# Kernel optimization log

Hardware: AMD Instinct MI355X
Metric: run time of the kernel (lower is better)

Reference implementation:

```python
import jax, jax.numpy as jnp
import numpy as np

B, N, K = 32, 65536, 2  # batch, nodes, residual dim per node


def setup_inputs() -> dict:
    key = jax.random.key(0)
    k0, k1, k2, k3, k4 = jax.random.split(key, 5)
    r = jax.random.normal(k0, (B, N, K), dtype=jnp.float32)
    w = jax.random.uniform(k1, (B, N, 2), dtype=jnp.float32)  # [conf, node_lambda]
    J_p = jax.random.normal(k2, (B, N, K, 6), dtype=jnp.float32)
    J_d = jax.random.normal(k3, (B, N, K, 1), dtype=jnp.float32)
    lmbda = jax.random.uniform(k4, (1, 1, 1), dtype=jnp.float32)
    return {"r": r, "w": w, "J_p": J_p, "J_d": J_d, "lmbda": lmbda}


def reference(r, w, J_p, J_d, lmbda):
    conf = w[..., 0:1][..., None]          # (B,N,1,1)
    node_lambda = w[..., 1:2]              # (B,N,1)

    cJp = conf * J_p                       # (B,N,K,6)
    cJd = conf * J_d                       # (B,N,K,1)

    H_pp = jnp.einsum('bnki,bnkj->bij', J_p, cJp)              # (B,6,6)
    H_pd = jnp.einsum('bnki,bnkj->bnij', J_p, cJd)             # (B,N,6,1)
    H_dd = jnp.einsum('bnk,bnk->bn', J_d[..., 0], cJd[..., 0])[..., None]  # (B,N,1)

    cr = conf[..., 0] * r                  # (B,N,K)
    g_p = jnp.einsum('bnki,bnk->bi', J_p, cr)[..., None]       # (B,6,1)
    g_d = jnp.einsum('bnk,bnk->bn', J_d[..., 0], cr)[..., None]  # (B,N,1)

    eye6 = jnp.eye(6, dtype=r.dtype)[None]                     # (1,6,6)
    H_pp = H_pp + lmbda * eye6
    H_dd = H_dd + lmbda + node_lambda                          # (B,N,1)

    inv_H_dd = 1.0 / (H_dd + 1e-6)                             # (B,N,1)
    H_pd_inv = H_pd * inv_H_dd[..., None]                      # (B,N,6,1)

    # Schur complement: H_eff = H_pp - sum_n H_pd * inv(H_dd) * H_pd^T
    H_eff = H_pp - jnp.einsum('bnik,bnjk->bij', H_pd_inv, H_pd)  # (B,6,6)
    H_eff = 0.5 * (H_eff + jnp.swapaxes(H_eff, -1, -2))
    H_eff = H_eff + 1e-3 * eye6

    g_eff = g_p - jnp.sum(H_pd_inv * g_d[..., None], axis=1)   # (B,6,1)

    delta_pose = jnp.linalg.solve(H_eff, g_eff)                # (B,6,1)

    # back-substitution for depth updates
    v = jnp.einsum('bnik,bi->bnk', H_pd, delta_pose[..., 0])   # (B,N,1)
    delta_depth = inv_H_dd * (g_d - v)                          # (B,N,1)

    return delta_pose[..., 0], delta_depth
```

## Files before the change

### kernel.cpp

```cpp
#include <hip/hip_runtime.h>

#define BN_B 32
#define BN_N 65536
#define BLOCKS_PER_B 64
#define THREADS 256

typedef _Float16 half_t;
struct alignas(16) Half8 { half_t h[8]; };
union StateU { Half8 s; uint4 u; };

#define STATE_OFFSET (256 * 1024)
#define STATE_BYTES ((size_t)BN_B * BN_N * 16)
#define WS_NEEDED (STATE_OFFSET + STATE_BYTES)

__device__ __forceinline__ void point_core(
    const float* __restrict__ r, const float* __restrict__ w,
    const float* __restrict__ J_p, const float* __restrict__ J_d,
    size_t p, float lam,
    float jpa[6], float jpb[6], float& c, float& cr0, float& cr1,
    float hpd[6], float& gd, float& ihdd)
{
    float2 wv = *(const float2*)(w + p * 2);
    float2 rv = *(const float2*)(r + p * 2);
    float2 jd = *(const float2*)(J_d + p * 2);
    float4 jp0 = *(const float4*)(J_p + p * 12);
    float4 jp1 = *(const float4*)(J_p + p * 12 + 4);
    float4 jp2 = *(const float4*)(J_p + p * 12 + 8);
    c = wv.x;
    float nl = wv.y;
    jpa[0] = jp0.x; jpa[1] = jp0.y; jpa[2] = jp0.z; jpa[3] = jp0.w; jpa[4] = jp1.x; jpa[5] = jp1.y;
    jpb[0] = jp1.z; jpb[1] = jp1.w; jpb[2] = jp2.x; jpb[3] = jp2.y; jpb[4] = jp2.z; jpb[5] = jp2.w;
    float cjd0 = c * jd.x, cjd1 = c * jd.y;
#pragma unroll
    for (int i = 0; i < 6; ++i) hpd[i] = jpa[i] * cjd0 + jpb[i] * cjd1;
    float hdd = jd.x * cjd0 + jd.y * cjd1;
    cr0 = c * rv.x; cr1 = c * rv.y;
    gd = jd.x * cr0 + jd.y * cr1;
    ihdd = 1.0f / (hdd + lam + nl + 1e-6f);
}

template <bool WRITE_STATE>
__global__ __launch_bounds__(THREADS) void k_reduce(
    const float* __restrict__ r, const float* __restrict__ w,
    const float* __restrict__ J_p, const float* __restrict__ J_d,
    const float* __restrict__ lmbda, float* __restrict__ partials,
    uint4* __restrict__ state)
{
    const int b = blockIdx.y;
    const int blk = blockIdx.x;
    const float lam = lmbda[0];

    float acc[27];
#pragma unroll
    for (int i = 0; i < 27; ++i) acc[i] = 0.0f;

    const int n0 = blk * (BN_N / BLOCKS_PER_B);
    const int n1 = n0 + (BN_N / BLOCKS_PER_B);
    const size_t baseP = (size_t)b * BN_N;

    for (int n = n0 + (int)threadIdx.x; n < n1; n += THREADS) {
        size_t p = baseP + n;
        float jpa[6], jpb[6], hpd[6];
        float c, cr0, cr1, gd, ihdd;
        point_core(r, w, J_p, J_d, p, lam, jpa, jpb, c, cr0, cr1, hpd, gd, ihdd);

        StateU su;
        int t = 0;
#pragma unroll
        for (int i = 0; i < 6; ++i) {
            float ca = c * jpa[i];
            float cb = c * jpb[i];
            float hs = ihdd * hpd[i];
#pragma unroll
            for (int j = i; j < 6; ++j, ++t)
                acc[t] += ca * jpa[j] + cb * jpb[j] - hs * hpd[j];
            acc[21 + i] += jpa[i] * cr0 + jpb[i] * cr1 - hs * gd;
            if (WRITE_STATE) su.s.h[i] = (half_t)hs;
        }
        if (WRITE_STATE) {
            su.s.h[6] = (half_t)(ihdd * gd);
            su.s.h[7] = (half_t)0.0f;
            state[p] = su.u;
        }
    }

#pragma unroll
    for (int i = 0; i < 27; ++i) {
        float v = acc[i];
#pragma unroll
        for (int off = 32; off > 0; off >>= 1) v += __shfl_down(v, off);
        acc[i] = v;
    }

    __shared__ float red[4][27];
    const int wave = threadIdx.x >> 6;
    const int lane = threadIdx.x & 63;
    if (lane == 0) {
#pragma unroll
        for (int i = 0; i < 27; ++i) red[wave][i] = acc[i];
    }
    __syncthreads();
    if (threadIdx.x < 27) {
        float s = red[0][threadIdx.x] + red[1][threadIdx.x] +
                  red[2][threadIdx.x] + red[3][threadIdx.x];
        partials[((size_t)b * BLOCKS_PER_B + blk) * 27 + threadIdx.x] = s;
    }
}

__global__ void k_solve(const float* __restrict__ partials,
                        const float* __restrict__ lmbda,
                        float* __restrict__ out)
{
    const int b = blockIdx.x;
    __shared__ float sum27[27];
    if (threadIdx.x < 27) {
        float s = 0.0f;
        for (int p = 0; p < BLOCKS_PER_B; ++p)
            s += partials[((size_t)b * BLOCKS_PER_B + p) * 27 + threadIdx.x];
        sum27[threadIdx.x] = s;
    }
    __syncthreads();
    if (threadIdx.x == 0) {
        const float lam = lmbda[0];
        float A[6][7];
        int t = 0;
        for (int i = 0; i < 6; ++i)
            for (int j = i; j < 6; ++j, ++t) { A[i][j] = sum27[t]; A[j][i] = sum27[t]; }
        for (int i = 0; i < 6; ++i) A[i][i] += lam + 0.001f;
        for (int i = 0; i < 6; ++i) A[i][6] = sum27[21 + i];

        for (int col = 0; col < 6; ++col) {
            int piv = col;
            float best = fabsf(A[col][col]);
            for (int rw = col + 1; rw < 6; ++rw) {
                float v = fabsf(A[rw][col]);
                if (v > best) { best = v; piv = rw; }
            }
            if (piv != col) {
                for (int j = 0; j < 7; ++j) {
                    float tmp = A[col][j]; A[col][j] = A[piv][j]; A[piv][j] = tmp;
                }
            }
            float inv = 1.0f / A[col][col];
            for (int rw = col + 1; rw < 6; ++rw) {
                float f = A[rw][col] * inv;
                for (int j = col; j < 7; ++j) A[rw][j] -= f * A[col][j];
            }
        }
        float x[6];
        for (int i = 5; i >= 0; --i) {
            float s = A[i][6];
            for (int j = i + 1; j < 6; ++j) s -= A[i][j] * x[j];
            x[i] = s / A[i][i];
        }
        for (int i = 0; i < 6; ++i) out[b * 6 + i] = x[i];
    }
}

__global__ __launch_bounds__(THREADS) void k_depth2(
    const uint4* __restrict__ state, const float* __restrict__ dp,
    float* __restrict__ out_depth)
{
    const int b = blockIdx.y;
    const int blk = blockIdx.x;
    float d[6];
#pragma unroll
    for (int i = 0; i < 6; ++i) d[i] = dp[b * 6 + i];

    const int n0 = blk * (BN_N / BLOCKS_PER_B);
    const int n1 = n0 + (BN_N / BLOCKS_PER_B);
    const size_t baseP = (size_t)b * BN_N;

    for (int n = n0 + (int)threadIdx.x; n < n1; n += THREADS) {
        size_t p = baseP + n;
        StateU su;
        su.u = state[p];
        float v = 0.0f;
#pragma unroll
        for (int i = 0; i < 6; ++i) v += (float)su.s.h[i] * d[i];
        out_depth[p] = (float)su.s.h[6] - v;
    }
}

__global__ __launch_bounds__(THREADS) void k_depth(
    const float* __restrict__ r, const float* __restrict__ w,
    const float* __restrict__ J_p, const float* __restrict__ J_d,
    const float* __restrict__ lmbda, const float* __restrict__ dp,
    float* __restrict__ out_depth)
{
    const int b = blockIdx.y;
    const int blk = blockIdx.x;
    const float lam = lmbda[0];
    float d0 = dp[b * 6 + 0], d1 = dp[b * 6 + 1], d2 = dp[b * 6 + 2];
    float d3 = dp[b * 6 + 3], d4 = dp[b * 6 + 4], d5 = dp[b * 6 + 5];

    const int n0 = blk * (BN_N / BLOCKS_PER_B);
    const int n1 = n0 + (BN_N / BLOCKS_PER_B);
    const size_t baseP = (size_t)b * BN_N;

    for (int n = n0 + (int)threadIdx.x; n < n1; n += THREADS) {
        size_t p = baseP + n;
        float jpa[6], jpb[6], hpd[6];
        float c, cr0, cr1, gd, ihdd;
        point_core(r, w, J_p, J_d, p, lam, jpa, jpb, c, cr0, cr1, hpd, gd, ihdd);
        float v = hpd[0] * d0 + hpd[1] * d1 + hpd[2] * d2 +
                  hpd[3] * d3 + hpd[4] * d4 + hpd[5] * d5;
        out_depth[p] = ihdd * (gd - v);
    }
}

extern "C" void kernel_launch(void* const* d_in, const int* in_sizes, int n_in,
                              void* d_out, int out_size, void* d_ws, size_t ws_size,
                              hipStream_t stream) {
    const float* r     = (const float*)d_in[0];
    const float* w     = (const float*)d_in[1];
    const float* J_p   = (const float*)d_in[2];
    const float* J_d   = (const float*)d_in[3];
    const float* lmbda = (const float*)d_in[4];
    float* out = (float*)d_out;
    float* partials = (float*)d_ws;
    uint4* state = (uint4*)((char*)d_ws + STATE_OFFSET);

    dim3 grid(BLOCKS_PER_B, BN_B);
    if (ws_size >= WS_NEEDED) {
        k_reduce<true><<<grid, THREADS, 0, stream>>>(r, w, J_p, J_d, lmbda, partials, state);
        k_solve<<<dim3(BN_B), 32, 0, stream>>>(partials, lmbda, out);
        k_depth2<<<grid, THREADS, 0, stream>>>(state, out, out + 192);
    } else {
        k_reduce<false><<<grid, THREADS, 0, stream>>>(r, w, J_p, J_d, lmbda, partials, nullptr);
        k_solve<<<dim3(BN_B), 32, 0, stream>>>(partials, lmbda, out);
        k_depth<<<grid, THREADS, 0, stream>>>(r, w, J_p, J_d, lmbda, out, out + 192);
    }
}
```

Measured before the change: 51.59 us.

## Fuse pose solve into reduction via last-block atomic counter

Removes the separate solve kernel: each reduction block writes its partial sums, bumps a per-batch atomic counter, and the last block to finish sums the partials and runs the 6x6 solve. The point loops are fully unrolled over a fixed per-thread count, and the half-precision state is packed with explicit pair packing. This drops one kernel launch and its dependency gap. In exchange it adds a memset launch to reset the counters, plus atomic and fence overhead.

```diff
diff --git a/kernel.cpp b/kernel.cpp
--- a/kernel.cpp
+++ b/kernel.cpp
@@ -2,16 +2,24 @@
 
 #define BN_B 32
 #define BN_N 65536
+#define THREADS 256
 #define BLOCKS_PER_B 64
-#define THREADS 256
+#define PTS_PER_BLOCK (BN_N / BLOCKS_PER_B)
+#define PTS_PER_THREAD (PTS_PER_BLOCK / THREADS)
+
+#define CNT_OFF (256 * 1024)
+#define STATE_OFF (512 * 1024)
+#define STATE_BYTES ((size_t)BN_B * BN_N * 16)
+#define WS_NEEDED (STATE_OFF + STATE_BYTES)
 
 typedef _Float16 half_t;
+union HPack { half_t h[2]; unsigned int u; };
 struct alignas(16) Half8 { half_t h[8]; };
 union StateU { Half8 s; uint4 u; };
 
-#define STATE_OFFSET (256 * 1024)
-#define STATE_BYTES ((size_t)BN_B * BN_N * 16)
-#define WS_NEEDED (STATE_OFFSET + STATE_BYTES)
+__device__ __forceinline__ unsigned int packh(float a, float b) {
+    HPack p; p.h[0] = (half_t)a; p.h[1] = (half_t)b; return p.u;
+}
 
 __device__ __forceinline__ void point_core(
     const float* __restrict__ r, const float* __restrict__ w,
@@ -39,48 +47,77 @@
     ihdd = 1.0f / (hdd + lam + nl + 1e-6f);
 }
 
+__device__ __forceinline__ void solve6(volatile float As[6][7], float x[6]) {
+    for (int col = 0; col < 6; ++col) {
+        int piv = col;
+        float best = fabsf(As[col][col]);
+        for (int rw = col + 1; rw < 6; ++rw) {
+            float v = fabsf(As[rw][col]);
+            if (v > best) { best = v; piv = rw; }
+        }
+        if (piv != col) {
+            for (int j = 0; j < 7; ++j) {
+                float tmp = As[col][j]; As[col][j] = As[piv][j]; As[piv][j] = tmp;
+            }
+        }
+        float inv = 1.0f / As[col][col];
+        for (int rw = col + 1; rw < 6; ++rw) {
+            float f = As[rw][col] * inv;
+            for (int j = col; j < 7; ++j) As[rw][j] -= f * As[col][j];
+        }
+    }
+    for (int i = 5; i >= 0; --i) {
+        float s = As[i][6];
+        for (int j = i + 1; j < 6; ++j) s -= As[i][j] * x[j];
+        x[i] = s / As[i][i];
+    }
+}
+
 template <bool WRITE_STATE>
-__global__ __launch_bounds__(THREADS) void k_reduce(
+__global__ __launch_bounds__(THREADS) void k_reduce_solve(
     const float* __restrict__ r, const float* __restrict__ w,
     const float* __restrict__ J_p, const float* __restrict__ J_d,
-    const float* __restrict__ lmbda, float* __restrict__ partials,
-    uint4* __restrict__ state)
-{
-    const int b = blockIdx.y;
+    const float* __restrict__ lmbda, char* __restrict__ ws,
+    float* __restrict__ out)
+{
+    float* partials = (float*)ws;
+    int*   cnt      = (int*)(ws + CNT_OFF);
+    uint4* state    = (uint4*)(ws + STATE_OFF);
+
+    const int b   = blockIdx.y;
     const int blk = blockIdx.x;
     const float lam = lmbda[0];
+    const size_t base = (size_t)b * BN_N + (size_t)blk * PTS_PER_BLOCK + threadIdx.x;
 
     float acc[27];
 #pragma unroll
     for (int i = 0; i < 27; ++i) acc[i] = 0.0f;
 
-    const int n0 = blk * (BN_N / BLOCKS_PER_B);
-    const int n1 = n0 + (BN_N / BLOCKS_PER_B);
-    const size_t baseP = (size_t)b * BN_N;
-
-    for (int n = n0 + (int)threadIdx.x; n < n1; n += THREADS) {
-        size_t p = baseP + n;
+#pragma unroll
+    for (int kk = 0; kk < PTS_PER_THREAD; ++kk) {
+        const size_t p = base + (size_t)kk * THREADS;
         float jpa[6], jpb[6], hpd[6];
         float c, cr0, cr1, gd, ihdd;
         point_core(r, w, J_p, J_d, p, lam, jpa, jpb, c, cr0, cr1, hpd, gd, ihdd);
-
-        StateU su;
+        float hs[6];
         int t = 0;
 #pragma unroll
         for (int i = 0; i < 6; ++i) {
             float ca = c * jpa[i];
             float cb = c * jpb[i];
-            float hs = ihdd * hpd[i];
+            hs[i] = ihdd * hpd[i];
 #pragma unroll
             for (int j = i; j < 6; ++j, ++t)
-                acc[t] += ca * jpa[j] + cb * jpb[j] - hs * hpd[j];
-            acc[21 + i] += jpa[i] * cr0 + jpb[i] * cr1 - hs * gd;
-            if (WRITE_STATE) su.s.h[i] = (half_t)hs;
+                acc[t] += ca * jpa[j] + cb * jpb[j] - hs[i] * hpd[j];
+            acc[21 + i] += jpa[i] * cr0 + jpb[i] * cr1 - hs[i] * gd;
         }
         if (WRITE_STATE) {
-            su.s.h[6] = (half_t)(ihdd * gd);
-            su.s.h[7] = (half_t)0.0f;
-            state[p] = su.u;
+            uint4 su;
+            su.x = packh(hs[0], hs[1]);
+            su.y = packh(hs[2], hs[3]);
+            su.z = packh(hs[4], hs[5]);
+            su.w = packh(ihdd * gd, 0.0f);
+            state[p] = su;
         }
     }
 
@@ -93,67 +130,49 @@
     }
 
     __shared__ float red[4][27];
-    const int wave = threadIdx.x >> 6;
-    const int lane = threadIdx.x & 63;
-    if (lane == 0) {
-#pragma unroll
-        for (int i = 0; i < 27; ++i) red[wave][i] = acc[i];
+    __shared__ float As[6][7];
+    __shared__ int amLast;
+    {
+        const int wave = threadIdx.x >> 6;
+        const int lane = threadIdx.x & 63;
+        if (lane == 0) {
+#pragma unroll
+            for (int i = 0; i < 27; ++i) red[wave][i] = acc[i];
+        }
     }
     __syncthreads();
     if (threadIdx.x < 27) {
-        float s = red[0][threadIdx.x] + red[1][threadIdx.x] +
-                  red[2][threadIdx.x] + red[3][threadIdx.x];
-        partials[((size_t)b * BLOCKS_PER_B + blk) * 27 + threadIdx.x] = s;
-    }
-}
-
-__global__ void k_solve(const float* __restrict__ partials,
-                        const float* __restrict__ lmbda,
-                        float* __restrict__ out)
-{
-    const int b = blockIdx.x;
-    __shared__ float sum27[27];
-    if (threadIdx.x < 27) {
-        float s = 0.0f;
-        for (int p = 0; p < BLOCKS_PER_B; ++p)
-            s += partials[((size_t)b * BLOCKS_PER_B + p) * 27 + threadIdx.x];
-        sum27[threadIdx.x] = s;
+        partials[((size_t)b * BLOCKS_PER_B + blk) * 27 + threadIdx.x] =
+            red[0][threadIdx.x] + red[1][threadIdx.x] +
+            red[2][threadIdx.x] + red[3][threadIdx.x];
     }
     __syncthreads();
     if (threadIdx.x == 0) {
-        const float lam = lmbda[0];
-        float A[6][7];
-        int t = 0;
-        for (int i = 0; i < 6; ++i)
-            for (int j = i; j < 6; ++j, ++t) { A[i][j] = sum27[t]; A[j][i] = sum27[t]; }
-        for (int i = 0; i < 6; ++i) A[i][i] += lam + 0.001f;
-        for (int i = 0; i < 6; ++i) A[i][6] = sum27[21 + i];
-
-        for (int col = 0; col < 6; ++col) {
-            int piv = col;
-            float best = fabsf(A[col][col]);
-            for (int rw = col + 1; rw < 6; ++rw) {
-                float v = fabsf(A[rw][col]);
-                if (v > best) { best = v; piv = rw; }
-            }
-            if (piv != col) {
-                for (int j = 0; j < 7; ++j) {
-                    float tmp = A[col][j]; A[col][j] = A[piv][j]; A[piv][j] = tmp;
-                }
-            }
-            float inv = 1.0f / A[col][col];
-            for (int rw = col + 1; rw < 6; ++rw) {
-                float f = A[rw][col] * inv;
-                for (int j = col; j < 7; ++j) A[rw][j] -= f * A[col][j];
-            }
-        }
-        float x[6];
-        for (int i = 5; i >= 0; --i) {
-            float s = A[i][6];
-            for (int j = i + 1; j < 6; ++j) s -= A[i][j] * x[j];
-            x[i] = s / A[i][i];
-        }
-        for (int i = 0; i < 6; ++i) out[b * 6 + i] = x[i];
+        int old = __hip_atomic_fetch_add(&cnt[b * 32], 1, __ATOMIC_ACQ_REL,
+                                         __HIP_MEMORY_SCOPE_AGENT);
+        amLast = (old == BLOCKS_PER_B - 1);
+    }
+    __syncthreads();
+
+    if (amLast) {
+        __builtin_amdgcn_fence(__ATOMIC_ACQUIRE, "agent");
+        if (threadIdx.x < 27) {
+            float s = 0.0f;
+            for (int c2 = 0; c2 < BLOCKS_PER_B; ++c2)
+                s += partials[((size_t)b * BLOCKS_PER_B + c2) * 27 + threadIdx.x];
+            red[0][threadIdx.x] = s;
+        }
+        __syncthreads();
+        if (threadIdx.x == 0) {
+            int t = 0;
+            for (int i = 0; i < 6; ++i)
+                for (int j = i; j < 6; ++j, ++t) { As[i][j] = red[0][t]; As[j][i] = red[0][t]; }
+            for (int i = 0; i < 6; ++i) As[i][i] += lam + 0.001f;
+            for (int i = 0; i < 6; ++i) As[i][6] = red[0][21 + i];
+            float x[6];
+            solve6(As, x);
+            for (int i = 0; i < 6; ++i) out[b * 6 + i] = x[i];
+        }
     }
 }
 
@@ -167,12 +186,11 @@
 #pragma unroll
     for (int i = 0; i < 6; ++i) d[i] = dp[b * 6 + i];
 
-    const int n0 = blk * (BN_N / BLOCKS_PER_B);
-    const int n1 = n0 + (BN_N / BLOCKS_PER_B);
-    const size_t baseP = (size_t)b * BN_N;
-
-    for (int n = n0 + (int)threadIdx.x; n < n1; n += THREADS) {
-        size_t p = baseP + n;
+    const size_t base = (size_t)b * BN_N + (size_t)blk * PTS_PER_BLOCK + threadIdx.x;
+
+#pragma unroll
+    for (int kk = 0; kk < PTS_PER_THREAD; ++kk) {
+        const size_t p = base + (size_t)kk * THREADS;
         StateU su;
         su.u = state[p];
         float v = 0.0f;
@@ -182,7 +200,7 @@
     }
 }
 
-__global__ __launch_bounds__(THREADS) void k_depth(
+__global__ __launch_bounds__(THREADS) void k_depth_rc(
     const float* __restrict__ r, const float* __restrict__ w,
     const float* __restrict__ J_p, const float* __restrict__ J_d,
     const float* __restrict__ lmbda, const float* __restrict__ dp,
@@ -191,20 +209,19 @@
     const int b = blockIdx.y;
     const int blk = blockIdx.x;
     const float lam = lmbda[0];
-    float d0 = dp[b * 6 + 0], d1 = dp[b * 6 + 1], d2 = dp[b * 6 + 2];
-    float d3 = dp[b * 6 + 3], d4 = dp[b * 6 + 4], d5 = dp[b * 6 + 5];
-
-    const int n0 = blk * (BN_N / BLOCKS_PER_B);
-    const int n1 = n0 + (BN_N / BLOCKS_PER_B);
-    const size_t baseP = (size_t)b * BN_N;
-
-    for (int n = n0 + (int)threadIdx.x; n < n1; n += THREADS) {
-        size_t p = baseP + n;
+    float d[6];
+#pragma unroll
+    for (int i = 0; i < 6; ++i) d[i] = dp[b * 6 + i];
+
+    const size_t base = (size_t)b * BN_N + (size_t)blk * PTS_PER_BLOCK + threadIdx.x;
+#pragma unroll
+    for (int kk = 0; kk < PTS_PER_THREAD; ++kk) {
+        const size_t p = base + (size_t)kk * THREADS;
         float jpa[6], jpb[6], hpd[6];
         float c, cr0, cr1, gd, ihdd;
         point_core(r, w, J_p, J_d, p, lam, jpa, jpb, c, cr0, cr1, hpd, gd, ihdd);
-        float v = hpd[0] * d0 + hpd[1] * d1 + hpd[2] * d2 +
-                  hpd[3] * d3 + hpd[4] * d4 + hpd[5] * d5;
+        float v = hpd[0] * d[0] + hpd[1] * d[1] + hpd[2] * d[2] +
+                  hpd[3] * d[3] + hpd[4] * d[4] + hpd[5] * d[5];
         out_depth[p] = ihdd * (gd - v);
     }
 }
@@ -218,17 +235,16 @@
     const float* J_d   = (const float*)d_in[3];
     const float* lmbda = (const float*)d_in[4];
     float* out = (float*)d_out;
-    float* partials = (float*)d_ws;
-    uint4* state = (uint4*)((char*)d_ws + STATE_OFFSET);
+    char* ws = (char*)d_ws;
+
+    hipMemsetAsync(ws + CNT_OFF, 0, 4096, stream);
 
     dim3 grid(BLOCKS_PER_B, BN_B);
     if (ws_size >= WS_NEEDED) {
-        k_reduce<true><<<grid, THREADS, 0, stream>>>(r, w, J_p, J_d, lmbda, partials, state);
-        k_solve<<<dim3(BN_B), 32, 0, stream>>>(partials, lmbda, out);
-        k_depth2<<<grid, THREADS, 0, stream>>>(state, out, out + 192);
+        k_reduce_solve<true><<<grid, THREADS, 0, stream>>>(r, w, J_p, J_d, lmbda, ws, out);
+        k_depth2<<<grid, THREADS, 0, stream>>>((uint4*)(ws + STATE_OFF), out, out + 192);
     } else {
-        k_reduce<false><<<grid, THREADS, 0, stream>>>(r, w, J_p, J_d, lmbda, partials, nullptr);
-        k_solve<<<dim3(BN_B), 32, 0, stream>>>(partials, lmbda, out);
-        k_depth<<<grid, THREADS, 0, stream>>>(r, w, J_p, J_d, lmbda, out, out + 192);
-    }
-}
+        k_reduce_solve<false><<<grid, THREADS, 0, stream>>>(r, w, J_p, J_d, lmbda, ws, out);
+        k_depth_rc<<<grid, THREADS, 0, stream>>>(r, w, J_p, J_d, lmbda, out, out + 192);
+    }
+}
```

Result: slower. 116.0 us (+124.8%).
